# Kernel tuning notes

Measured on AMD Instinct MI355X. Metric: run time of the kernel, lower is better.

The kernel has to match this reference:

```python
import jax, jax.numpy as jnp
import numpy as np
import math

B, S, DIM = 1, 2048, 2048
H, KVH, HD = 32, 8, 64
REP = H // KVH


def _rope_cache(seqlen, head_dim, base=10000.0):
    # (seqlen, 2*head_dim): [cos | sin], each duplicated across both halves
    inv_freq = 1.0 / (base ** (np.arange(0, head_dim, 2, dtype=np.float32) / head_dim))
    t = np.arange(seqlen, dtype=np.float32)
    ang = np.outer(t, inv_freq)                    # (S, HD/2)
    ang = np.concatenate([ang, ang], axis=-1)      # (S, HD)
    return jnp.asarray(np.concatenate([np.cos(ang), np.sin(ang)], axis=-1))


def setup_inputs() -> dict:
    key = jax.random.key(0)
    ks = jax.random.split(key, 12)
    std = 0.02
    return {
        "x": jax.random.normal(ks[0], (B, S, DIM), jnp.float32),
        "rope_cache": _rope_cache(S, HD),
        "wq_w": jax.random.normal(ks[1], (H * HD, DIM), jnp.float32) * std,
        "wq_b": jax.random.normal(ks[2], (H * HD,), jnp.float32) * std,
        "wk_w": jax.random.normal(ks[3], (KVH * HD, DIM), jnp.float32) * std,
        "wk_b": jax.random.normal(ks[4], (KVH * HD,), jnp.float32) * std,
        "wv_w": jax.random.normal(ks[5], (KVH * HD, DIM), jnp.float32) * std,
        "wv_b": jax.random.normal(ks[6], (KVH * HD,), jnp.float32) * std,
        "wo_w": jax.random.normal(ks[7], (DIM, H * HD), jnp.float32) * std,
        "wo_b": jax.random.normal(ks[8], (DIM,), jnp.float32) * std,
        "sinks": jax.random.normal(ks[9], (H,), jnp.float32) * std,
    }


def _rotate_half(t):
    h = t.shape[-1] // 2
    return jnp.concatenate([-t[..., h:], t[..., :h]], axis=-1)


def reference(x, rope_cache, wq_w, wq_b, wk_w, wk_b, wv_w, wv_b, wo_w, wo_b, sinks):
    bsz, seqlen, _ = x.shape
    q = (jnp.einsum('bsd,od->bso', x, wq_w) + wq_b).reshape(bsz, seqlen, H, HD)
    k = (jnp.einsum('bsd,od->bso', x, wk_w) + wk_b).reshape(bsz, seqlen, KVH, HD)
    v = (jnp.einsum('bsd,od->bso', x, wv_w) + wv_b).reshape(bsz, seqlen, KVH, HD)

    cos = rope_cache[:seqlen, :HD][None, :, None, :]
    sin = rope_cache[:seqlen, HD:][None, :, None, :]
    q = q * cos + _rotate_half(q) * sin
    k = k * cos + _rotate_half(k) * sin

    # repeat_kv: repeat_interleave along head dim
    k = jnp.repeat(k, REP, axis=2)  # (B,S,H,HD)
    v = jnp.repeat(v, REP, axis=2)

    q = q.transpose(0, 2, 1, 3)  # (B,H,S,HD)
    k = k.transpose(0, 2, 1, 3)
    v = v.transpose(0, 2, 1, 3)

    scale = 1.0 / math.sqrt(HD)
    scores = jnp.einsum('bhqd,bhkd->bhqk', q, k) * scale
    causal = jnp.tril(jnp.ones((seqlen, seqlen), dtype=bool))
    scores = jnp.where(causal, scores, -jnp.inf)

    m = jnp.max(scores, axis=-1, keepdims=True)
    lse = m[..., 0] + jnp.log(jnp.sum(jnp.exp(scores - m), axis=-1))  # (B,H,S)
    attn = jnp.exp(scores - lse[..., None])
    out = jnp.einsum('bhqk,bhkd->bhqd', attn, v)

    # sink-token LSE renormalization
    combined_lse = jnp.logaddexp(lse, sinks[None, :, None])
    renorm = jnp.exp(jnp.clip(lse - combined_lse, -20.0, 0.0))
    out = out * renorm[..., None]

    out = out.transpose(0, 2, 1, 3).reshape(bsz, seqlen, H * HD)
    return jnp.einsum('bso,do->bsd', out, wo_w) + wo_b
```

## Files before the change

kernel.cpp:

```cpp
#include <hip/hip_runtime.h>


#define S_LEN 2048
#define DIM_  2048
#define QK_LD 2560

typedef __attribute__((ext_vector_type(8))) __bf16 bf16x8;
typedef __attribute__((ext_vector_type(4))) float f32x4;
typedef __attribute__((ext_vector_type(4))) unsigned short us4;

__device__ __forceinline__ unsigned short f2bf(float f) {
    const __bf16 h = (__bf16)f;
    return __builtin_bit_cast(unsigned short, h);
}
__device__ __forceinline__ float bf2f(unsigned short u) {
    union { unsigned u; float f; } v; v.u = ((unsigned)u) << 16;
    return v.f;
}

__device__ __forceinline__ void gload_lds16(const void* g, void* l) {
    __builtin_amdgcn_global_load_lds(
        (const __attribute__((address_space(1))) void*)g,
        (__attribute__((address_space(3))) void*)l, 16, 0, 0);
}

__device__ __forceinline__ int swz32(int r, int ch) { return r*32 + ((ch ^ ((r >> 1) & 3)) << 3); }
__device__ __forceinline__ int swz64(int r, int ch) { return r*64 + ((ch ^ (r & 7)) << 3); }

__global__ void cvt_all(const float* __restrict__ x,  const float* __restrict__ wq,
                        const float* __restrict__ wk, const float* __restrict__ wv,
                        const float* __restrict__ wo,
                        unsigned short* __restrict__ xb,
                        unsigned short* __restrict__ wqkv,
                        unsigned short* __restrict__ wob) {
    const int i4 = blockIdx.x * 256 + threadIdx.x;
    const float* src; unsigned short* dst; int off;
    if (i4 < 1048576)      { src = x;  dst = xb;             off = i4; }
    else if (i4 < 2097152) { src = wq; dst = wqkv;           off = i4 - 1048576; }
    else if (i4 < 2359296) { src = wk; dst = wqkv + 4194304; off = i4 - 2097152; }
    else if (i4 < 2621440) { src = wv; dst = wqkv + 5242880; off = i4 - 2359296; }
    else                   { src = wo; dst = wob;            off = i4 - 2621440; }
    const float4 v = reinterpret_cast<const float4*>(src)[off];
    us4 o = { f2bf(v.x), f2bf(v.y), f2bf(v.z), f2bf(v.w) };
    reinterpret_cast<us4*>(dst)[off] = o;
}

__global__ void build_bias(const float* __restrict__ qb, const float* __restrict__ kb,
                           const float* __restrict__ vb, float* __restrict__ out) {
    const int i = blockIdx.x * 256 + threadIdx.x;
    if (i < 2048) out[i] = qb[i];
    else if (i < 2560) out[i] = kb[i - 2048];
    else if (i < 3072) out[i] = vb[i - 2560];
}

__global__ __launch_bounds__(256)
void gemm_part(const unsigned short* __restrict__ A,
               const unsigned short* __restrict__ B,
               unsigned short* __restrict__ P,
               int K, int ldc)
{
    __shared__ unsigned short As[2][128 * 32];
    __shared__ unsigned short Bs[2][128 * 32];
    const int t = threadIdx.x;
    const int lane = t & 63;
    const int w = t >> 6;
    const int wr = w >> 1, wc = w & 1;
    const int lq = lane & 15;
    const int g = lane >> 4;
    const int m0 = blockIdx.y * 128;
    const int n0 = blockIdx.x * 128;
    const int kbase = blockIdx.z * (K >> 1);
    const size_t zoff = (size_t)blockIdx.z * 2048 * ldc;

    const f32x4 z = {0.f, 0.f, 0.f, 0.f};
    f32x4 acc[4][4];
    #pragma unroll
    for (int i = 0; i < 4; i++)
        #pragma unroll
        for (int j = 0; j < 4; j++) acc[i][j] = z;

    auto stage = [&](int buf, int k0) {
        #pragma unroll
        for (int c = 0; c < 2; c++) {
            const int chunk = w * 128 + c * 64 + lane;
            const int r = chunk >> 2;
            const int chl = (chunk & 3) ^ ((r >> 1) & 3);
            gload_lds16(&A[(size_t)(m0 + r) * K + kbase + k0 + (chl << 3)],
                        &As[buf][(size_t)(w * 128 + c * 64) * 8]);
            gload_lds16(&B[(size_t)(n0 + r) * K + kbase + k0 + (chl << 3)],
                        &Bs[buf][(size_t)(w * 128 + c * 64) * 8]);
        }
    };

    const int NIT = K >> 6;
    stage(0, 0);
    for (int it = 0; it < NIT; ++it) {
        const int cur = it & 1;
        asm volatile("s_waitcnt vmcnt(0)" ::: "memory");
        __builtin_amdgcn_s_barrier();
        if (it + 1 < NIT) stage(cur ^ 1, (it + 1) << 5);
        bf16x8 a[4], b[4];
        #pragma unroll
        for (int mi = 0; mi < 4; mi++)
            a[mi] = *reinterpret_cast<const bf16x8*>(&As[cur][swz32(wr * 64 + mi * 16 + lq, g)]);
        #pragma unroll
        for (int ni = 0; ni < 4; ni++)
            b[ni] = *reinterpret_cast<const bf16x8*>(&Bs[cur][swz32(wc * 64 + ni * 16 + lq, g)]);
        #pragma unroll
        for (int mi = 0; mi < 4; mi++)
            #pragma unroll
            for (int ni = 0; ni < 4; ni++)
                acc[mi][ni] = __builtin_amdgcn_mfma_f32_16x16x32_bf16(a[mi], b[ni], acc[mi][ni], 0, 0, 0);
    }

    #pragma unroll
    for (int mi = 0; mi < 4; mi++) {
        const int row0 = m0 + wr * 64 + mi * 16 + g * 4;
        #pragma unroll
        for (int ni = 0; ni < 4; ni++) {
            const int col = n0 + wc * 64 + ni * 16 + lq;
            #pragma unroll
            for (int j = 0; j < 4; j++)
                P[zoff + (size_t)(row0 + j) * ldc + col] = f2bf(acc[mi][ni][j]);
        }
    }
}

__global__ void rope_combine(const unsigned short* __restrict__ pq,
                             const float* __restrict__ bias,
                             const float* __restrict__ rope,
                             unsigned short* __restrict__ qk,
                             unsigned short* __restrict__ vt)
{
    const int idx = blockIdx.x * 256 + threadIdx.x;
    if (idx < 2621440) {
        const int s = idx / 1280;
        const int rem = idx - s * 1280;
        const int head = rem >> 5;
        const int p = rem & 31;
        const int col0 = head * 64 + p;
        const int col1 = col0 + 32;
        const size_t r0 = (size_t)s * 3072;
        const float v0 = bf2f(pq[r0 + col0]) + bf2f(pq[6291456 + r0 + col0]) + bias[col0];
        const float v1 = bf2f(pq[r0 + col1]) + bf2f(pq[6291456 + r0 + col1]) + bias[col1];
        const float c = rope[s * 128 + p];
        const float sn = rope[s * 128 + 64 + p];
        const float qs = (head < 32) ? 0.1803368801f : 1.0f;
        qk[(size_t)s * QK_LD + col0] = f2bf((v0 * c - v1 * sn) * qs);
        qk[(size_t)s * QK_LD + col1] = f2bf((v1 * c + v0 * sn) * qs);
    } else {
        const int i = idx - 2621440;
        const int d = i >> 9;
        const int s4 = (i & 511) << 2;
        const float bv = bias[2560 + d];
        us4 o;
        #pragma unroll
        for (int j = 0; j < 4; j++) {
            const size_t r = (size_t)(s4 + j) * 3072 + 2560 + d;
            o[j] = f2bf(bf2f(pq[r]) + bf2f(pq[6291456 + r]) + bv);
        }
        *reinterpret_cast<us4*>(&vt[(size_t)d * S_LEN + s4]) = o;
    }
}

__global__ __launch_bounds__(256)
void attn_kernel(const unsigned short* __restrict__ qk,
                 const unsigned short* __restrict__ vt,
                 unsigned short* __restrict__ pacc,
                 float* __restrict__ pml)
{
    const int h = blockIdx.x;
    const int by = blockIdx.y;
    const int c = by & 1;
    const int qb = 31 - (by >> 1);
    const int hkv = h >> 2;
    const int t = threadIdx.x;
    const int lane = t & 63;
    const int w = t >> 6;
    const int lq = lane & 15;
    const int g = lane >> 4;

    __shared__ unsigned short Ks[2][64 * 64];
    __shared__ unsigned short Vs[2][64 * 64];
    __shared__ unsigned short Ps[4][16 * 64];
    unsigned short* Pw = &Ps[w][0];

    const int qrow = qb * 64 + w * 16 + lq;

    bf16x8 aq[2];
    #pragma unroll
    for (int cc = 0; cc < 2; cc++)
        aq[cc] = *reinterpret_cast<const bf16x8*>(&qk[(size_t)qrow * QK_LD + h * 64 + cc * 32 + g * 8]);
    {
        const uint4 u0 = reinterpret_cast<const uint4&>(aq[0]);
        const uint4 u1 = reinterpret_cast<const uint4&>(aq[1]);
        asm volatile("" :: "v"(u0.x), "v"(u0.y), "v"(u0.z), "v"(u0.w),
                           "v"(u1.x), "v"(u1.y), "v"(u1.z), "v"(u1.w));
    }

    const f32x4 z = {0.f, 0.f, 0.f, 0.f};
    f32x4 acc[4];
    #pragma unroll
    for (int df = 0; df < 4; df++) acc[df] = z;
    float m = -1e30f, l = 0.f;

    auto stage = [&](int buf, int tv) {
        const int kv0 = tv * 64;
        #pragma unroll
        for (int i = 0; i < 2; i++) {
            const int chunk = i * 256 + w * 64 + lane;
            const int r = chunk >> 3;
            const int chl = (chunk & 7) ^ (r & 7);
            gload_lds16(&qk[(size_t)(kv0 + r) * QK_LD + 2048 + hkv * 64 + (chl << 3)],
                        &Ks[buf][(size_t)(i * 256 + w * 64) * 8]);
            gload_lds16(&vt[(size_t)(hkv * 64 + r) * S_LEN + kv0 + (chl << 3)],
                        &Vs[buf][(size_t)(i * 256 + w * 64) * 8]);
        }
    };

    const int ntile = (qb >= c) ? ((qb - c) >> 1) + 1 : 0;
    if (ntile > 0) stage(0, c);
    int cur = 0;
    for (int i = 0; i < ntile; ++i) {
        const int tv = c + 2 * i;
        asm volatile("s_waitcnt vmcnt(0)" ::: "memory");
        __builtin_amdgcn_s_barrier();
        if (i + 1 < ntile) stage(cur ^ 1, tv + 2);

        f32x4 sc[4];
        #pragma unroll
        for (int f = 0; f < 4; f++) {
            sc[f] = z;
            #pragma unroll
            for (int cc = 0; cc < 2; cc++) {
                const bf16x8 bk = *reinterpret_cast<const bf16x8*>(&Ks[cur][swz64(f * 16 + lq, cc * 4 + g)]);
                sc[f] = __builtin_amdgcn_mfma_f32_16x16x32_bf16(bk, aq[cc], sc[f], 0, 0, 0);
            }
        }

        if (tv == qb) {
            const int thr = w * 16 + lq - g * 4;
            #pragma unroll
            for (int f = 0; f < 4; f++)
                #pragma unroll
                for (int j = 0; j < 4; j++)
                    if (f * 16 + j > thr) sc[f][j] = -1e30f;
        }

        float mx = sc[0][0];
        #pragma unroll
        for (int f = 0; f < 4; f++)
            #pragma unroll
            for (int j = 0; j < 4; j++) mx = fmaxf(mx, sc[f][j]);
        mx = fmaxf(mx, __shfl_xor(mx, 16));
        mx = fmaxf(mx, __shfl_xor(mx, 32));
        const float mn = fmaxf(m, mx);
        const float rs = exp2f(m - mn);
        m = mn;
        float s = 0.f;
        #pragma unroll
        for (int f = 0; f < 4; f++)
            #pragma unroll
            for (int j = 0; j < 4; j++) {
                const float p = exp2f(sc[f][j] - mn);
                sc[f][j] = p;
                s += p;
            }
        s += __shfl_xor(s, 16);
        s += __shfl_xor(s, 32);
        l = l * rs + s;
        #pragma unroll
        for (int df = 0; df < 4; df++) acc[df] *= rs;

        #pragma unroll
        for (int f = 0; f < 4; f++) {
            us4 pk = { f2bf(sc[f][0]), f2bf(sc[f][1]), f2bf(sc[f][2]), f2bf(sc[f][3]) };
            *reinterpret_cast<us4*>(
                &Pw[lq * 64 + ((((f << 1) | (g >> 1)) ^ (lq & 7)) << 3) + ((g & 1) << 2)]) = pk;
        }
        #pragma unroll
        for (int cc = 0; cc < 2; cc++) {
            const bf16x8 pb = *reinterpret_cast<const bf16x8*>(
                &Pw[lq * 64 + (((cc * 4 + g) ^ (lq & 7)) << 3)]);
            #pragma unroll
            for (int df = 0; df < 4; df++) {
                const bf16x8 bv = *reinterpret_cast<const bf16x8*>(&Vs[cur][swz64(df * 16 + lq, cc * 4 + g)]);
                acc[df] = __builtin_amdgcn_mfma_f32_16x16x32_bf16(bv, pb, acc[df], 0, 0, 0);
            }
        }
        cur ^= 1;
    }

    const size_t rbase = ((size_t)(h * 2 + c) * 2048 + qrow);
    #pragma unroll
    for (int df = 0; df < 4; df++) {
        us4 pk = { f2bf(acc[df][0]), f2bf(acc[df][1]), f2bf(acc[df][2]), f2bf(acc[df][3]) };
        *reinterpret_cast<us4*>(&pacc[rbase * 64 + df * 16 + g * 4]) = pk;
    }
    if (g == 0) {
        pml[rbase * 2]     = m;
        pml[rbase * 2 + 1] = l;
    }
}

__global__ void attn_combine(const unsigned short* __restrict__ pacc,
                             const float* __restrict__ pml,
                             const float* __restrict__ sinks,
                             unsigned short* __restrict__ abuf) {
    const int idx = blockIdx.x * 256 + threadIdx.x;
    const int q4 = idx & 3;
    const int row = (idx >> 2) & 2047;
    const int h = idx >> 13;
    const size_t r0 = (size_t)(h * 2 + 0) * 2048 + row;
    const size_t r1 = (size_t)(h * 2 + 1) * 2048 + row;
    const float m0 = pml[r0 * 2], l0 = pml[r0 * 2 + 1];
    const float m1 = pml[r1 * 2], l1 = pml[r1 * 2 + 1];
    const float M = fmaxf(m0, m1);
    const float w0 = exp2f(m0 - M), w1 = exp2f(m1 - M);
    const float L = l0 * w0 + l1 * w1;
    const float lse = 0.6931471806f * (M + log2f(L));
    const float d = sinks[h] - lse;
    float f = (d > 20.f) ? d : log1pf(__expf(d));
    if (f > 20.f) f = 20.f;
    const float fac = __expf(-f) / L;
    const unsigned short* a0 = &pacc[r0 * 64 + q4 * 16];
    const unsigned short* a1 = &pacc[r1 * 64 + q4 * 16];
    unsigned short* dst = &abuf[(size_t)row * DIM_ + h * 64 + q4 * 16];
    #pragma unroll
    for (int k = 0; k < 4; k++) {
        const us4 x0 = *reinterpret_cast<const us4*>(&a0[k * 4]);
        const us4 x1 = *reinterpret_cast<const us4*>(&a1[k * 4]);
        us4 r;
        #pragma unroll
        for (int j = 0; j < 4; j++)
            r[j] = f2bf((bf2f(x0[j]) * w0 + bf2f(x1[j]) * w1) * fac);
        *reinterpret_cast<us4*>(&dst[k * 4]) = r;
    }
}

__global__ void o_combine(const unsigned short* __restrict__ po,
                          const float* __restrict__ ob,
                          float* __restrict__ out) {
    const int idx = blockIdx.x * 256 + threadIdx.x;
    const int row = idx >> 9;
    const int c4 = (idx & 511) << 2;
    float4 o;
    const size_t r = (size_t)row * 2048 + c4;
    const us4 x0 = *reinterpret_cast<const us4*>(&po[r]);
    const us4 x1 = *reinterpret_cast<const us4*>(&po[4194304 + r]);
    o.x = bf2f(x0[0]) + bf2f(x1[0]) + ob[c4];
    o.y = bf2f(x0[1]) + bf2f(x1[1]) + ob[c4 + 1];
    o.z = bf2f(x0[2]) + bf2f(x1[2]) + ob[c4 + 2];
    o.w = bf2f(x0[3]) + bf2f(x1[3]) + ob[c4 + 3];
    *reinterpret_cast<float4*>(&out[r]) = o;
}

extern "C" void kernel_launch(void* const* d_in, const int* in_sizes, int n_in,
                              void* d_out, int out_size, void* d_ws, size_t ws_size,
                              hipStream_t stream) {
    const float* x     = (const float*)d_in[0];
    const float* rope  = (const float*)d_in[1];
    const float* wq_w  = (const float*)d_in[2];
    const float* wq_b  = (const float*)d_in[3];
    const float* wk_w  = (const float*)d_in[4];
    const float* wk_b  = (const float*)d_in[5];
    const float* wv_w  = (const float*)d_in[6];
    const float* wv_b  = (const float*)d_in[7];
    const float* wo_w  = (const float*)d_in[8];
    const float* wo_b  = (const float*)d_in[9];
    const float* sinks = (const float*)d_in[10];
    float* out = (float*)d_out;

    char* ws = (char*)d_ws;
    unsigned short* xb    = (unsigned short*)(ws);
    unsigned short* wqkv  = (unsigned short*)(ws + (8u  << 20));
    unsigned short* wob   = (unsigned short*)(ws + (20u << 20));
    unsigned short* pq    = (unsigned short*)(ws + (28u << 20));
    unsigned short* qkbuf = (unsigned short*)(ws);
    unsigned short* vtbuf = (unsigned short*)(ws + (10u << 20));
    unsigned short* pacc  = (unsigned short*)(ws + (28u << 20));
    float*          pml   = (float*)(ws + (44u << 20));
    unsigned short* abuf  = (unsigned short*)(ws + (46u << 20));
    unsigned short* po    = (unsigned short*)(ws);
    float*          bcat  = (float*)(ws + (54u << 20));

    cvt_all<<<14336, 256, 0, stream>>>(x, wq_w, wk_w, wv_w, wo_w, xb, wqkv, wob);
    build_bias<<<12, 256, 0, stream>>>(wq_b, wk_b, wv_b, bcat);

    gemm_part<<<dim3(24, 16, 2), 256, 0, stream>>>(xb, wqkv, pq, 2048, 3072);
    rope_combine<<<11264, 256, 0, stream>>>(pq, bcat, rope, qkbuf, vtbuf);
    attn_kernel<<<dim3(32, 64), 256, 0, stream>>>(qkbuf, vtbuf, pacc, pml);
    attn_combine<<<1024, 256, 0, stream>>>(pacc, pml, sinks, abuf);
    gemm_part<<<dim3(16, 16, 2), 256, 0, stream>>>(abuf, wob, po, 2048, 2048);
    o_combine<<<4096, 256, 0, stream>>>(po, wo_b, out);
}
```

Baseline: 252.6 us.

## Use 128-row query blocks with 8 waves sharing each staged K/V tile

The attention kernel now launches 512-thread blocks covering 128 query rows, so each K/V tile loaded into LDS is reused by eight waves instead of four, halving the global K/V traffic per query. The causal mask is applied per wave via a vote on row thresholds, using -inf. Online-softmax rescaling is skipped when no lane's running max increases. The tail after the loop (not shown) must agree with the new qp indexing, and larger blocks may reduce occupancy and make the causal diagonal work less balanced.

After: 257.5 us. No clear change (+1.9%).

```diff
diff --git a/kernel.cpp b/kernel.cpp
--- a/kernel.cpp
+++ b/kernel.cpp
@@ -163,16 +163,16 @@
     }
 }
 
-__global__ __launch_bounds__(256)
+__global__ __launch_bounds__(512)
 void attn_kernel(const unsigned short* __restrict__ qk,
                  const unsigned short* __restrict__ vt,
                  unsigned short* __restrict__ pacc,
                  float* __restrict__ pml)
 {
     const int h = blockIdx.x;
-    const int by = blockIdx.y;
-    const int c = by & 1;
-    const int qb = 31 - (by >> 1);
+    const int qc = blockIdx.y;
+    const int c = qc & 1;
+    const int qp = 15 - (qc >> 1);
     const int hkv = h >> 2;
     const int t = threadIdx.x;
     const int lane = t & 63;
@@ -182,10 +182,10 @@
 
     __shared__ unsigned short Ks[2][64 * 64];
     __shared__ unsigned short Vs[2][64 * 64];
-    __shared__ unsigned short Ps[4][16 * 64];
+    __shared__ unsigned short Ps[8][16 * 64];
     unsigned short* Pw = &Ps[w][0];
 
-    const int qrow = qb * 64 + w * 16 + lq;
+    const int qrow = qp * 128 + w * 16 + lq;
 
     bf16x8 aq[2];
     #pragma unroll
@@ -206,20 +206,16 @@
 
     auto stage = [&](int buf, int tv) {
         const int kv0 = tv * 64;
-        #pragma unroll
-        for (int i = 0; i < 2; i++) {
-            const int chunk = i * 256 + w * 64 + lane;
-            const int r = chunk >> 3;
-            const int chl = (chunk & 7) ^ (r & 7);
-            gload_lds16(&qk[(size_t)(kv0 + r) * QK_LD + 2048 + hkv * 64 + (chl << 3)],
-                        &Ks[buf][(size_t)(i * 256 + w * 64) * 8]);
-            gload_lds16(&vt[(size_t)(hkv * 64 + r) * S_LEN + kv0 + (chl << 3)],
-                        &Vs[buf][(size_t)(i * 256 + w * 64) * 8]);
-        }
+        const int r = t >> 3;
+        const int chl = (t & 7) ^ (r & 7);
+        gload_lds16(&qk[(size_t)(kv0 + r) * QK_LD + 2048 + hkv * 64 + (chl << 3)],
+                    &Ks[buf][(size_t)w * 512]);
+        gload_lds16(&vt[(size_t)(hkv * 64 + r) * S_LEN + kv0 + (chl << 3)],
+                    &Vs[buf][(size_t)w * 512]);
     };
 
-    const int ntile = (qb >= c) ? ((qb - c) >> 1) + 1 : 0;
-    if (ntile > 0) stage(0, c);
+    const int ntile = qp + 1;
+    stage(0, c);
     int cur = 0;
     for (int i = 0; i < ntile; ++i) {
         const int tv = c + 2 * i;
@@ -238,13 +234,13 @@
             }
         }
 
-        if (tv == qb) {
-            const int thr = w * 16 + lq - g * 4;
+        const int thr = qrow - tv * 64 - g * 4;
+        if (__any(thr < 51)) {
             #pragma unroll
             for (int f = 0; f < 4; f++)
                 #pragma unroll
                 for (int j = 0; j < 4; j++)
-                    if (f * 16 + j > thr) sc[f][j] = -1e30f;
+                    if (f * 16 + j > thr) sc[f][j] = -__builtin_inff();
         }
 
         float mx = sc[0][0];
@@ -254,9 +250,9 @@
             for (int j = 0; j < 4; j++) mx = fmaxf(mx, sc[f][j]);
         mx = fmaxf(mx, __shfl_xor(mx, 16));
         mx = fmaxf(mx, __shfl_xor(mx, 32));
-        const float mn = fmaxf(m, mx);
-        const float rs = exp2f(m - mn);
-        m = mn;
+
+        const bool need = !__all(mx <= m);
+        const float mn = need ? fmaxf(m, mx) : m;
         float s = 0.f;
         #pragma unroll
         for (int f = 0; f < 4; f++)
@@ -268,9 +264,15 @@
             }
         s += __shfl_xor(s, 16);
         s += __shfl_xor(s, 32);
-        l = l * rs + s;
-        #pragma unroll
-        for (int df = 0; df < 4; df++) acc[df] *= rs;
+        if (need) {
+            const float rs = exp2f(m - mn);
+            m = mn;
+            l = l * rs + s;
+            #pragma unroll
+            for (int df = 0; df < 4; df++) acc[df] *= rs;
+        } else {
+            l += s;
+        }
 
         #pragma unroll
         for (int f = 0; f < 4; f++) {
@@ -389,7 +391,7 @@
 
     gemm_part<<<dim3(24, 16, 2), 256, 0, stream>>>(xb, wqkv, pq, 2048, 3072);
     rope_combine<<<11264, 256, 0, stream>>>(pq, bcat, rope, qkbuf, vtbuf);
-    attn_kernel<<<dim3(32, 64), 256, 0, stream>>>(qkbuf, vtbuf, pacc, pml);
+    attn_kernel<<<dim3(32, 32), 512, 0, stream>>>(qkbuf, vtbuf, pacc, pml);
     attn_combine<<<1024, 256, 0, stream>>>(pacc, pml, sinks, abuf);
     gemm_part<<<dim3(16, 16, 2), 256, 0, stream>>>(abuf, wob, po, 2048, 2048);
     o_combine<<<4096, 256, 0, stream>>>(po, wo_b, out);
```
